# Kernel tuning notes

Hardware: AMD Instinct MI355X
Metric: run time of the kernel (lower is better)

The kernel has to match this reference:

```python
import jax, jax.numpy as jnp
import numpy as np

B = 1024
N_ATOMS = 51
FLAT = 7 * 7 * 64  # conv output: 84->20->9->7 spatial, 64 channels


def _conv(x, w, b, s):
    # x: NCHW, w: OIHW, VALID padding, stride s
    y = jax.lax.conv_general_dilated(
        x, w, window_strides=(s, s), padding='VALID',
        dimension_numbers=('NCHW', 'OIHW', 'NCHW'))
    return y + b[None, :, None, None]


def setup_inputs() -> dict:
    key = jax.random.key(0)
    ks = jax.random.split(key, 8)

    def w(k, shape, fan_in):
        return jax.random.normal(k, shape, dtype=jnp.float32) / np.float32(np.sqrt(fan_in))

    return {
        'x': jax.random.uniform(ks[0], (B, 4, 84, 84), jnp.float32, 0.0, 256.0),
        'cw1': w(ks[1], (32, 4, 8, 8), 4 * 8 * 8), 'cb1': jnp.zeros((32,), jnp.float32),
        'cw2': w(ks[2], (64, 32, 4, 4), 32 * 4 * 4), 'cb2': jnp.zeros((64,), jnp.float32),
        'cw3': w(ks[3], (64, 64, 3, 3), 64 * 3 * 3), 'cb3': jnp.zeros((64,), jnp.float32),
        'fw1': w(ks[4], (FLAT, 256), FLAT), 'fb1': jnp.zeros((256,), jnp.float32),
        'fw2': w(ks[5], (256, N_ATOMS), 256), 'fb2': jnp.zeros((N_ATOMS,), jnp.float32),
        'z': jnp.linspace(-10.0, 10.0, N_ATOMS).astype(jnp.float32),  # support atoms
        'n_out': 6,
    }


def reference(x, cw1, cb1, cw2, cb2, cw3, cb3, fw1, fb1, fw2, fb2, z, n_out):
    x = x / 256.0
    x = jax.nn.relu(_conv(x, cw1, cb1, 4))  # [B,32,20,20]
    x = jax.nn.relu(_conv(x, cw2, cb2, 2))  # [B,64,9,9]
    x = jax.nn.relu(_conv(x, cw3, cb3, 1))  # [B,64,7,7]
    h = x.reshape(x.shape[0], -1)           # [B,3136]
    h = jax.nn.relu(h @ fw1 + fb1)          # [B,256]
    p = jax.nn.softmax(h @ fw2 + fb2, axis=1)  # [B,n_atoms]
    # Original loop writes fc_layers(x)[i] identically for every action j:
    dist = jnp.broadcast_to(p[:, None, :], (p.shape[0], n_out, p.shape[1]))
    res = jnp.einsum('bna,a->bn', dist, z)  # expected value per action
    return (dist, res)
```

## Files before the change

kernel.cpp:

```cpp
#include <hip/hip_runtime.h>
#include <hip/hip_fp16.h>

#define RL(x) __builtin_amdgcn_readfirstlane(x)

typedef _Float16 f16x8 __attribute__((ext_vector_type(8)));
typedef _Float16 f16x4 __attribute__((ext_vector_type(4)));
typedef float    f32x16 __attribute__((ext_vector_type(16)));

__global__ __launch_bounds__(256) void wprep_k(const float* __restrict__ w1,
                                               const float* __restrict__ w2,
                                               const float* __restrict__ w3,
                                               __half* __restrict__ w1h,
                                               __half* __restrict__ w2h,
                                               float* __restrict__ wt3) {
  int i = blockIdx.x * 256 + threadIdx.x;
  if (i < 8192) {
    int kx = i & 7, oc = (i >> 3) & 31, ky = (i >> 8) & 7, ic = i >> 11;
    w1h[i] = __float2half(w1[oc * 256 + ic * 64 + ky * 8 + kx]);
  }
  if (i < 32768) {
    int j = i & 7, ln = (i >> 3) & 31, kh = (i >> 8) & 1, ot = (i >> 9) & 1, ic = i >> 10;
    int k = kh * 8 + j, kx = k >> 2, ky = k & 3, oc = ot * 32 + ln;
    w2h[i] = __float2half(w2[oc * 512 + ic * 16 + ky * 4 + kx]);
  }
  if (i < 36864) {
    int o3 = i % 24, o = o3 / 3, kx = o3 - o * 3;
    int r = i / 24, ocg = r & 7, r2 = r >> 3, ky = r2 % 3, ic = r2 / 3;
    wt3[i] = w3[(ocg * 8 + o) * 576 + ic * 9 + ky * 3 + kx];
  }
}

__global__ __launch_bounds__(256, 2) void conv1_k(const float* __restrict__ x,
                                                  const __half* __restrict__ w1h,
                                                  const float* __restrict__ bias,
                                                  __half* __restrict__ out) {
  __shared__ __align__(16) __half xs[32256];
  const int bid = blockIdx.x;
  const int q  = bid % 10;
  const int bt = bid / 10;
  const int tid = threadIdx.x;
  const int lane = tid & 63;
  const int wv   = RL(tid >> 6);
  const int pyl = wv >> 1;
  const int pxq = wv & 1;
  const int kh = lane >> 5;
  const int ln = lane & 31;

  f32x16 acc[10];
#pragma unroll
  for (int px = 0; px < 10; ++px)
#pragma unroll
    for (int r = 0; r < 16; ++r) acc[px][r] = 0.f;

  const float inv = 1.0f / 256.0f;
  const float* xb = x + bt * 32 * 28224 + q * 8 * 84;

#pragma unroll 1
  for (int ic = 0; ic < 4; ++ic) {
    if (ic) __syncthreads();
#pragma unroll 4
    for (int pass = 0; pass < 32; ++pass) {
      int item = pass * 256 + tid;
      if (item < 8064) {
        int cg = item % 21;
        int rb = item / 21;
        int b = rb & 31, r = rb >> 5;
        const float* gp = xb + b * 28224 + ic * 7056 + r * 84 + cg * 4;
        float4 v = *(const float4*)gp;
        __half2 h01 = __floats2half2_rn(v.x * inv, v.y * inv);
        __half2 h23 = __floats2half2_rn(v.z * inv, v.w * inv);
        *(uint2*)&xs[(r * 32 + b) * 84 + cg * 4] =
            make_uint2(*(unsigned*)&h01, *(unsigned*)&h23);
      }
    }
    __syncthreads();

#pragma unroll
    for (int t = 0; t < 4; ++t) {
      f16x8 aw = *(const f16x8*)(w1h + ((ic * 8 + 2 * t + kh) * 32 + ln) * 8);
      const __half* rp = &xs[((pyl * 4 + 2 * t + kh) * 32 + ln) * 84];
#pragma unroll
      for (int px = 0; px < 10; ++px) {
        const int xg = pxq * 10 + px;
        f16x4 lo = *(const f16x4*)(rp + 4 * xg);
        f16x4 hi = *(const f16x4*)(rp + 4 * xg + 4);
        f16x8 bx;
        bx[0]=lo[0]; bx[1]=lo[1]; bx[2]=lo[2]; bx[3]=lo[3];
        bx[4]=hi[0]; bx[5]=hi[1]; bx[6]=hi[2]; bx[7]=hi[3];
        acc[px] = __builtin_amdgcn_mfma_f32_32x32x16_f16(aw, bx, acc[px], 0, 0, 0);
      }
    }
  }

  float bv[16];
#pragma unroll
  for (int r = 0; r < 16; ++r)
    bv[r] = bias[(r & 3) + 8 * (r >> 2) + 4 * kh];

  const int pyg = 2 * q + pyl;
  const int bg  = bt * 32 + ln;
#pragma unroll
  for (int px = 0; px < 10; ++px) {
    const int p = pyg * 20 + pxq * 10 + px;
#pragma unroll
    for (int r = 0; r < 16; ++r) {
      const int oc = (r & 3) + 8 * (r >> 2) + 4 * kh;
      float v = acc[px][r] + bv[r];
      out[(oc * 400 + p) * 1024 + bg] = __float2half(v > 0.f ? v : 0.f);
    }
  }
}

__global__ __launch_bounds__(256, 1) void conv2_k(const __half* __restrict__ in,
                                                  const __half* __restrict__ w2h,
                                                  const float* __restrict__ bias,
                                                  __half* __restrict__ out) {
  __shared__ __align__(16) __half sh[2][9216];
  const int bid = blockIdx.x;
  const int opy = bid % 9;
  const int bt  = bid / 9;
  const int bbase = bt * 64;
  const int tid  = threadIdx.x;
  const int lane = tid & 63;
  const int wv   = RL(tid >> 6);
  const int octile = wv & 1;
  const int bsub   = wv >> 1;
  const int kh = lane >> 5;
  const int ln = lane & 31;

  const unsigned short* inu = (const unsigned short*)in;
  const unsigned short* wu  = (const unsigned short*)w2h;

  int roff[5], offA[5];
#pragma unroll
  for (int p = 0; p < 5; ++p) {
    int idx = p * 256 + tid;
    int px = idx >> 6, b = idx & 63;
    roff[p] = px * 1024 + b;
    offA[p] = b * 128 + ((((px >> 1) ^ (b & 7)) << 3) | ((px & 1) << 2));
  }
  const int base0 = (40 * opy) * 1024 + bbase;

  f32x16 acc[9];
#pragma unroll
  for (int ox = 0; ox < 9; ++ox)
#pragma unroll
    for (int r = 0; r < 16; ++r) acc[ox][r] = 0.f;

  ushort4 s0, s1, s2, s3, s4; uint2 sW;

#define C2_LOAD(icv) do {                                                     \
    const unsigned short* ibp = inu + (icv) * 409600 + base0;                 \
    s0 = make_ushort4(ibp[roff[0]], ibp[roff[0]+20480], ibp[roff[0]+40960], ibp[roff[0]+61440]); \
    s1 = make_ushort4(ibp[roff[1]], ibp[roff[1]+20480], ibp[roff[1]+40960], ibp[roff[1]+61440]); \
    s2 = make_ushort4(ibp[roff[2]], ibp[roff[2]+20480], ibp[roff[2]+40960], ibp[roff[2]+61440]); \
    s3 = make_ushort4(ibp[roff[3]], ibp[roff[3]+20480], ibp[roff[3]+40960], ibp[roff[3]+61440]); \
    s4 = make_ushort4(ibp[roff[4]], ibp[roff[4]+20480], ibp[roff[4]+40960], ibp[roff[4]+61440]); \
    sW = *(const uint2*)(wu + (icv) * 1024 + tid * 4);                        \
  } while (0)

#define C2_STORE(buf) do {                                                    \
    *(uint2*)&sh[buf][offA[0]] = make_uint2((unsigned)s0.x | ((unsigned)s0.y << 16), (unsigned)s0.z | ((unsigned)s0.w << 16)); \
    *(uint2*)&sh[buf][offA[1]] = make_uint2((unsigned)s1.x | ((unsigned)s1.y << 16), (unsigned)s1.z | ((unsigned)s1.w << 16)); \
    *(uint2*)&sh[buf][offA[2]] = make_uint2((unsigned)s2.x | ((unsigned)s2.y << 16), (unsigned)s2.z | ((unsigned)s2.w << 16)); \
    *(uint2*)&sh[buf][offA[3]] = make_uint2((unsigned)s3.x | ((unsigned)s3.y << 16), (unsigned)s3.z | ((unsigned)s3.w << 16)); \
    *(uint2*)&sh[buf][offA[4]] = make_uint2((unsigned)s4.x | ((unsigned)s4.y << 16), (unsigned)s4.z | ((unsigned)s4.w << 16)); \
    *(uint2*)&sh[buf][8192 + tid * 4] = sW;                                   \
  } while (0)

  const int offW = 8192 + octile * 512 + kh * 256 + ln * 8;
  const int bloc = bsub * 32 + ln;
  const int bx7  = bloc & 7;
  const int brow = bloc * 128;

  int cur = 0;
  C2_LOAD(0);
#pragma unroll 1
  for (int ic = 0; ic < 32; ++ic) {
    __syncthreads();
    C2_STORE(cur);
    const int icn = ic < 31 ? ic + 1 : 31;
    C2_LOAD(icn);
    __syncthreads();
    f16x8 aw = *(const f16x8*)&sh[cur][offW];
#pragma unroll
    for (int ox = 0; ox < 9; ++ox) {
      f16x8 bx = *(const f16x8*)&sh[cur][brow + (((ox + kh) ^ bx7) << 3)];
      acc[ox] = __builtin_amdgcn_mfma_f32_32x32x16_f16(aw, bx, acc[ox], 0, 0, 0);
    }
    cur ^= 1;
  }
#undef C2_LOAD
#undef C2_STORE

  float bv[16];
#pragma unroll
  for (int r = 0; r < 16; ++r)
    bv[r] = bias[octile * 32 + (r & 3) + 8 * (r >> 2) + 4 * kh];
  const int bout = bbase + bloc;
#pragma unroll
  for (int ox = 0; ox < 9; ++ox) {
#pragma unroll
    for (int r = 0; r < 16; ++r) {
      const int oc = octile * 32 + (r & 3) + 8 * (r >> 2) + 4 * kh;
      float v = acc[ox][r] + bv[r];
      out[(oc * 81 + opy * 9 + ox) * 1024 + bout] = __float2half(v > 0.f ? v : 0.f);
    }
  }
}

__global__ __launch_bounds__(128, 2) void conv3_k(const __half* __restrict__ in,
                                                  const float* __restrict__ wt,
                                                  const float* __restrict__ bias,
                                                  __half* __restrict__ out) {
  const int bid = blockIdx.x;
  const int ocg = (bid >> 3) & 15;
  const int grp = ((bid >> 7) << 3) | (bid & 7);
  const int opy = grp % 7;
  const int bg  = grp / 7;
  const int tid  = threadIdx.x;
  const int lane = tid & 63;
  const int wv   = RL(tid >> 6);

  float acc[4][7];
#pragma unroll
  for (int o = 0; o < 4; ++o)
#pragma unroll
    for (int ox = 0; ox < 7; ++ox) acc[o][ox] = 0.f;

  const __half* ib = in + bg * 64 + lane;
  const int ic0 = wv * 32;

#pragma unroll 1
  for (int ici = 0; ici < 32; ++ici) {
    const int ic = ic0 + ici;
#pragma unroll
    for (int ky = 0; ky < 3; ++ky) {
      const float* wp = wt + ((ic * 3 + ky) * 8 + (ocg >> 1)) * 24 + (ocg & 1) * 12;
      float wk[12];
#pragma unroll
      for (int q = 0; q < 12; ++q) wk[q] = wp[q];
      const __half* rp = ib + (ic * 81 + (opy + ky) * 9) * 1024;
      float iv[9];
#pragma unroll
      for (int q = 0; q < 9; ++q) iv[q] = __half2float(rp[q * 1024]);
#pragma unroll
      for (int o = 0; o < 4; ++o)
#pragma unroll
        for (int ox = 0; ox < 7; ++ox)
#pragma unroll
          for (int kx = 0; kx < 3; ++kx)
            acc[o][ox] = fmaf(iv[ox + kx], wk[o * 3 + kx], acc[o][ox]);
    }
  }

  __shared__ float red[4][7][64];
  if (wv == 1) {
#pragma unroll
    for (int o = 0; o < 4; ++o)
#pragma unroll
      for (int ox = 0; ox < 7; ++ox) red[o][ox][lane] = acc[o][ox];
  }
  __syncthreads();
  if (wv == 0) {
#pragma unroll
    for (int o = 0; o < 4; ++o) {
      const int oc = ocg * 4 + o;
      const float bj = bias[oc];
#pragma unroll
      for (int ox = 0; ox < 7; ++ox) {
        float v = acc[o][ox] + red[o][ox][lane] + bj;
        out[(oc * 49 + opy * 7 + ox) * 1024 + bg * 64 + lane] =
            __float2half(v > 0.f ? v : 0.f);
      }
    }
  }
}

__global__ __launch_bounds__(64, 2) void fc1a_k(const __half* __restrict__ a,
                                                const float* __restrict__ w,
                                                float* __restrict__ part) {
  const int bid = blockIdx.x;
  const int jg  = (bid >> 3) & 15;
  const int grp = ((bid >> 7) << 3) | (bid & 7);
  const int kc  = grp & 15;
  const int bg  = grp >> 4;
  const int lane = threadIdx.x;

  float acc[16];
#pragma unroll
  for (int j = 0; j < 16; ++j) acc[j] = 0.f;

  const __half* ap = a + kc * 196 * 1024 + bg * 64 + lane;
  const float* wp0 = w + kc * 196 * 256 + jg * 16;

#pragma unroll 4
  for (int k = 0; k < 196; ++k) {
    float av = __half2float(ap[k * 1024]);
    const float* wp = wp0 + k * 256;
#pragma unroll
    for (int j = 0; j < 16; ++j) acc[j] = fmaf(av, wp[j], acc[j]);
  }
#pragma unroll
  for (int j = 0; j < 16; ++j)
    part[(kc * 256 + jg * 16 + j) * 1024 + bg * 64 + lane] = acc[j];
}

__global__ __launch_bounds__(256) void fc1b_k(const float* __restrict__ part,
                                              const float* __restrict__ bias,
                                              float* __restrict__ h) {
  int idx = blockIdx.x * 256 + threadIdx.x;
  float s = bias[idx >> 10];
#pragma unroll
  for (int c = 0; c < 16; ++c) s += part[c * 262144 + idx];
  h[idx] = s > 0.f ? s : 0.f;
}

__global__ __launch_bounds__(256) void fc2_k(const float* __restrict__ h,
                                             const float* __restrict__ w,
                                             const float* __restrict__ bias,
                                             const float* __restrict__ z,
                                             float* __restrict__ dist,
                                             float* __restrict__ res) {
  __shared__ float wl[256 * 51];
  const int tid = threadIdx.x;
#pragma unroll
  for (int i = tid; i < 256 * 51; i += 256) wl[i] = w[i];
  __syncthreads();

  const int j   = tid & 63;
  const int b   = blockIdx.x * 4 + RL(tid >> 6);
  const int jc = j < 51 ? j : 50;
  float acc = bias[jc];
#pragma unroll 8
  for (int k = 0; k < 256; ++k)
    acc = fmaf(h[k * 1024 + b], wl[k * 51 + jc], acc);
  float logit = (j < 51) ? acc : -1e30f;
  float m = logit;
#pragma unroll
  for (int o = 32; o > 0; o >>= 1) m = fmaxf(m, __shfl_xor(m, o, 64));
  float e = (j < 51) ? __expf(logit - m) : 0.f;
  float ssum = e;
#pragma unroll
  for (int o = 32; o > 0; o >>= 1) ssum += __shfl_xor(ssum, o, 64);
  float p = e / ssum;
  float zv = (j < 51) ? z[jc] : 0.f;
  float rz = p * zv;
#pragma unroll
  for (int o = 32; o > 0; o >>= 1) rz += __shfl_xor(rz, o, 64);
  if (j < 51) {
    float* db = dist + b * 6 * 51 + j;
#pragma unroll
    for (int n = 0; n < 6; ++n) db[n * 51] = p;
  }
  if (j < 6) res[b * 6 + j] = rz;
}

extern "C" void kernel_launch(void* const* d_in, const int* in_sizes, int n_in,
                              void* d_out, int out_size, void* d_ws, size_t ws_size,
                              hipStream_t stream) {
  const float* x   = (const float*)d_in[0];
  const float* cw1 = (const float*)d_in[1];
  const float* cb1 = (const float*)d_in[2];
  const float* cw2 = (const float*)d_in[3];
  const float* cb2 = (const float*)d_in[4];
  const float* cw3 = (const float*)d_in[5];
  const float* cb3 = (const float*)d_in[6];
  const float* fw1 = (const float*)d_in[7];
  const float* fb1 = (const float*)d_in[8];
  const float* fw2 = (const float*)d_in[9];
  const float* fb2 = (const float*)d_in[10];
  const float* z   = (const float*)d_in[11];

  float* ws = (float*)d_ws;
  __half* c1t = (__half*)(ws + 6553600);
  __half* c2t = (__half*)(ws + 13107200);
  __half* c3t = (__half*)(ws + 15761408);
  float*  pw  = ws;
  float*  h_t = ws + 4194304;

  float*  wt3n = (float*)d_out;
  __half* w1h  = (__half*)((float*)d_out + 36864);
  __half* w2h  = (__half*)((float*)d_out + 45056);

  float* dist = (float*)d_out;
  float* res  = dist + 1024 * 6 * 51;

  wprep_k<<<144, 256, 0, stream>>>(cw1, cw2, cw3, w1h, w2h, wt3n);
  conv1_k<<<320, 256, 0, stream>>>(x, w1h, cb1, c1t);
  conv2_k<<<144, 256, 0, stream>>>(c1t, w2h, cb2, c2t);
  conv3_k<<<1792, 128, 0, stream>>>(c2t, wt3n, cb3, c3t);
  fc1a_k<<<4096, 64, 0, stream>>>(c3t, fw1, pw);
  fc1b_k<<<1024, 256, 0, stream>>>(pw, fb1, h_t);
  fc2_k<<<256, 256, 0, stream>>>(h_t, fw2, fb2, z, dist, res);
}
```

Baseline: 436.3 us.

## Load conv1 input directly from global, dropping the LDS staging

The first convolution no longer stages the input tile into shared memory with barriers. Each lane now reads its own fp32 input window straight from global memory and converts it to fp16 in registers just before the MFMA. The 1/256 input scaling is folded into the fp16 conv1 weights during weight prep. This removes the LDS writes, LDS reads and barriers, but overlapping windows are now re-read from global memory and served by cache, and per-lane loads with a per-batch stride coalesce poorly.

```diff
diff --git a/kernel.cpp b/kernel.cpp
--- a/kernel.cpp
+++ b/kernel.cpp
@@ -4,7 +4,6 @@
 #define RL(x) __builtin_amdgcn_readfirstlane(x)
 
 typedef _Float16 f16x8 __attribute__((ext_vector_type(8)));
-typedef _Float16 f16x4 __attribute__((ext_vector_type(4)));
 typedef float    f32x16 __attribute__((ext_vector_type(16)));
 
 __global__ __launch_bounds__(256) void wprep_k(const float* __restrict__ w1,
@@ -16,7 +15,7 @@
   int i = blockIdx.x * 256 + threadIdx.x;
   if (i < 8192) {
     int kx = i & 7, oc = (i >> 3) & 31, ky = (i >> 8) & 7, ic = i >> 11;
-    w1h[i] = __float2half(w1[oc * 256 + ic * 64 + ky * 8 + kx]);
+    w1h[i] = __float2half(w1[oc * 256 + ic * 64 + ky * 8 + kx] * 0.00390625f);
   }
   if (i < 32768) {
     int j = i & 7, ln = (i >> 3) & 31, kh = (i >> 8) & 1, ot = (i >> 9) & 1, ic = i >> 10;
@@ -34,7 +33,6 @@
                                                   const __half* __restrict__ w1h,
                                                   const float* __restrict__ bias,
                                                   __half* __restrict__ out) {
-  __shared__ __align__(16) __half xs[32256];
   const int bid = blockIdx.x;
   const int q  = bid % 10;
   const int bt = bid / 10;
@@ -52,41 +50,25 @@
 #pragma unroll
     for (int r = 0; r < 16; ++r) acc[px][r] = 0.f;
 
-  const float inv = 1.0f / 256.0f;
-  const float* xb = x + bt * 32 * 28224 + q * 8 * 84;
+  const float* xb = x + (bt * 32 + ln) * 28224 + (q * 8 + pyl * 4 + kh) * 84 + pxq * 40;
 
 #pragma unroll 1
   for (int ic = 0; ic < 4; ++ic) {
-    if (ic) __syncthreads();
-#pragma unroll 4
-    for (int pass = 0; pass < 32; ++pass) {
-      int item = pass * 256 + tid;
-      if (item < 8064) {
-        int cg = item % 21;
-        int rb = item / 21;
-        int b = rb & 31, r = rb >> 5;
-        const float* gp = xb + b * 28224 + ic * 7056 + r * 84 + cg * 4;
-        float4 v = *(const float4*)gp;
-        __half2 h01 = __floats2half2_rn(v.x * inv, v.y * inv);
-        __half2 h23 = __floats2half2_rn(v.z * inv, v.w * inv);
-        *(uint2*)&xs[(r * 32 + b) * 84 + cg * 4] =
-            make_uint2(*(unsigned*)&h01, *(unsigned*)&h23);
-      }
-    }
-    __syncthreads();
-
 #pragma unroll
     for (int t = 0; t < 4; ++t) {
       f16x8 aw = *(const f16x8*)(w1h + ((ic * 8 + 2 * t + kh) * 32 + ln) * 8);
-      const __half* rp = &xs[((pyl * 4 + 2 * t + kh) * 32 + ln) * 84];
+      const float* rp = xb + ic * 7056 + 2 * t * 84;
 #pragma unroll
       for (int px = 0; px < 10; ++px) {
-        const int xg = pxq * 10 + px;
-        f16x4 lo = *(const f16x4*)(rp + 4 * xg);
-        f16x4 hi = *(const f16x4*)(rp + 4 * xg + 4);
-        f16x8 bx;
-        bx[0]=lo[0]; bx[1]=lo[1]; bx[2]=lo[2]; bx[3]=lo[3];
-        bx[4]=hi[0]; bx[5]=hi[1]; bx[6]=hi[2]; bx[7]=hi[3];
+        float4 lo = *(const float4*)(rp + 4 * px);
+        float4 hi = *(const float4*)(rp + 4 * px + 4);
+        __half2 p0 = __floats2half2_rn(lo.x, lo.y);
+        __half2 p1 = __floats2half2_rn(lo.z, lo.w);
+        __half2 p2 = __floats2half2_rn(hi.x, hi.y);
+        __half2 p3 = __floats2half2_rn(hi.z, hi.w);
+        uint4 u = make_uint4(*(unsigned*)&p0, *(unsigned*)&p1,
+                             *(unsigned*)&p2, *(unsigned*)&p3);
+        f16x8 bx = *(f16x8*)&u;
         acc[px] = __builtin_amdgcn_mfma_f32_32x32x16_f16(aw, bx, acc[px], 0, 0, 0);
       }
     }
```

Measured after the change: 428.5 us. About the same (-1.8%).
